# Kernel tuning notes

Hardware: AMD Instinct MI355X
Metric: run time of the kernel (lower is better)

## Reference

```python
import jax, jax.numpy as jnp
import numpy as np
from jax import lax

DN = ('NCHW', 'OIHW', 'NCHW')


def _conv(x, w, pad):
    return lax.conv_general_dilated(x, w, (1, 1), [(pad, pad), (pad, pad)], dimension_numbers=DN)


def _bn(x, gamma, beta, mean, var, eps=1e-5):
    inv = gamma * lax.rsqrt(var + eps)
    return x * inv[None, :, None, None] + (beta - mean * inv)[None, :, None, None]


def _unfold(x, K, pad):
    # torch.nn.Unfold layout: channel-major, kernel positions fastest -> (B, C, K*K, H, W)
    B, C, H, W = x.shape
    p = lax.conv_general_dilated_patches(x, (K, K), (1, 1), [(pad, pad), (pad, pad)], dimension_numbers=DN)
    return p.reshape(B, C, K * K, H, W)


def setup_inputs() -> dict:
    key = jax.random.key(0)
    ks = jax.random.split(key, 16)
    B, C, H, W, K = 16, 64, 64, 64, 3
    d = {
        'x': jax.random.normal(ks[0], (B, C, H, W), jnp.float32),
        'wq': jax.random.normal(ks[1], (C, C, 1, 1), jnp.float32) * 0.1,
        'wk': jax.random.normal(ks[2], (C, C, K, K), jnp.float32) * 0.05,
        'wv': jax.random.normal(ks[3], (C, C, 1, 1), jnp.float32) * 0.1,
        'pos_h': jax.random.normal(ks[4], (C, K, 1), jnp.float32),
        'pos_w': jax.random.normal(ks[5], (C, 1, K), jnp.float32),
    }
    for i, nm in enumerate(['q', 'k', 'v', 'o']):
        d[nm + '_gamma'] = jnp.ones((C,), jnp.float32)
        d[nm + '_beta'] = jnp.zeros((C,), jnp.float32)
        d[nm + '_mean'] = jax.random.normal(ks[6 + i], (C,), jnp.float32) * 0.1
        d[nm + '_var'] = jax.random.uniform(ks[10 + i], (C,), jnp.float32, 0.5, 1.5)
    return d


def reference(x, wq, q_gamma, q_beta, q_mean, q_var,
              wk, k_gamma, k_beta, k_mean, k_var,
              wv, v_gamma, v_beta, v_mean, v_var,
              pos_h, pos_w, o_gamma, o_beta, o_mean, o_var):
    B, C, H, W = x.shape
    K = pos_h.shape[1]
    heads = C // 8
    cph = C // heads  # channels per head

    q = jax.nn.relu(_bn(_conv(x, wq, 0), q_gamma, q_beta, q_mean, q_var))
    k = jax.nn.relu(_bn(_conv(x, wk, K // 2), k_gamma, k_beta, k_mean, k_var))
    v = _bn(_conv(x, wv, 0), v_gamma, v_beta, v_mean, v_var)

    # local keys + positional bias: (B, C, K*K, H, W)
    unfold_k = _unfold(k, K, K // 2)
    pos = (pos_h + pos_w).reshape(1, C, K * K, 1, 1)
    kp = (unfold_k + pos).reshape(B, heads, cph, K * K, H, W)
    qh = q.reshape(B, heads, cph, 1, H, W)

    attn = (qh * kp).sum(axis=2)            # (B, heads, K*K, H, W)
    attn = jax.nn.softmax(attn, axis=2)

    # local aggregation (LocalConvolution): weights shared across cph channels per head
    uv = _unfold(v, K, (K - 1) // 2).reshape(B, heads, cph, K * K, H, W)
    out = (attn[:, :, None] * uv).sum(axis=3).reshape(B, C, H, W)

    out = jax.nn.relu(_bn(out, o_gamma, o_beta, o_mean, o_var))
    return out
```

## Files before the change

### kernel.cpp

```cpp
#include <hip/hip_runtime.h>
#include <hip/hip_bf16.h>
#include <math.h>

#define B_ 16
#define C_ 64
#define H_ 64
#define W_ 64
#define KSTEPS 18

typedef __attribute__((ext_vector_type(8))) short bf16x8;
typedef __attribute__((ext_vector_type(4))) short bf16x4;
typedef __attribute__((ext_vector_type(4))) float f32x4;

static __device__ __forceinline__ unsigned short f2b(float f) {
    __hip_bfloat16 h = __float2bfloat16(f);
    return *reinterpret_cast<unsigned short*>(&h);
}
static __device__ __forceinline__ float b2f(unsigned short u) {
    __hip_bfloat16 h;
    *reinterpret_cast<unsigned short*>(&h) = u;
    return __bfloat162float(h);
}

__global__ __launch_bounds__(64) void prep_kernel(
    const float* __restrict__ wq, const float* __restrict__ wk, const float* __restrict__ wv,
    const float* __restrict__ qg, const float* __restrict__ qb, const float* __restrict__ qm, const float* __restrict__ qv,
    const float* __restrict__ kg, const float* __restrict__ kb, const float* __restrict__ km, const float* __restrict__ kv,
    const float* __restrict__ vg, const float* __restrict__ vb, const float* __restrict__ vm, const float* __restrict__ vv,
    const float* __restrict__ og, const float* __restrict__ ob, const float* __restrict__ om, const float* __restrict__ ov,
    unsigned short* __restrict__ Wp, float* __restrict__ bnp)
{
    const int bid = blockIdx.x;
    const int lane = threadIdx.x;
    if (bid < 12 * KSTEPS) {
        const int mf = bid / KSTEPS;
        const int ks = bid % KSTEPS;
        const int r = lane & 15;
        bf16x8 u;
#pragma unroll
        for (int j = 0; j < 8; j++) {
            int k = ks * 32 + ((lane >> 4) << 3) + j;
            int tap = k >> 6;
            int c = k & 63;
            float w;
            if (mf < 4)      { int co = mf * 16 + r;        w = (tap == 4) ? wq[co * 64 + c] : 0.f; }
            else if (mf < 8) { int co = (mf - 4) * 16 + r;  w = wk[(co * 64 + c) * 9 + tap]; }
            else             { int co = (mf - 8) * 16 + r;  w = (tap == 4) ? wv[co * 64 + c] : 0.f; }
            u[j] = (short)f2b(w);
        }
        *reinterpret_cast<bf16x8*>(Wp + ((size_t)(mf * KSTEPS + ks) * 64 + lane) * 8) = u;
    } else {
        const int c = lane;
        const float* G[4] = {qg, kg, vg, og};
        const float* Bt[4] = {qb, kb, vb, ob};
        const float* M[4] = {qm, km, vm, om};
        const float* V[4] = {qv, kv, vv, ov};
#pragma unroll
        for (int p = 0; p < 4; p++) {
            float inv = G[p][c] * rsqrtf(V[p][c] + 1e-5f);
            bnp[p * 128 + c] = inv;
            bnp[p * 128 + 64 + c] = Bt[p][c] - M[p][c] * inv;
        }
    }
}

__global__ __launch_bounds__(256) void xt_kernel(
    const float* __restrict__ x, unsigned short* __restrict__ xt)
{
    __shared__ float ls[64][65];
    const int b = blockIdx.x >> 6;
    const int h = blockIdx.x & 63;
    const int tid = threadIdx.x;
    const int w = tid & 63;
    const int cg = tid >> 6;
#pragma unroll
    for (int cc = 0; cc < 16; cc++) {
        int c = cg * 16 + cc;
        ls[c][w] = x[((b * 64 + c) * 64 + h) * 64 + w];
    }
    __syncthreads();
    const int px = tid & 63;
    bf16x8 u0, u1;
#pragma unroll
    for (int j = 0; j < 8; j++) {
        u0[j] = (short)f2b(ls[cg * 16 + j][px]);
        u1[j] = (short)f2b(ls[cg * 16 + 8 + j][px]);
    }
    size_t base = ((size_t)((b * 64 + h) * 64 + px)) * 64 + cg * 16;
    *reinterpret_cast<bf16x8*>(xt + base) = u0;
    *reinterpret_cast<bf16x8*>(xt + base + 8) = u1;
}

#define KSM_OFF 0
#define VSM_OFF 25344
#define QSM_OFF 50688
__global__ __launch_bounds__(512, 2) void fused_kernel(
    const unsigned short* __restrict__ xt, const unsigned short* __restrict__ Wp,
    const float* __restrict__ bnp,
    const float* __restrict__ ph, const float* __restrict__ pw,
    float* __restrict__ out)
{
    __shared__ __align__(16) char smem[58880];
    __shared__ float bns[512];
    __shared__ float phs[192], pws[192];
    const int bid = blockIdx.x;
    const int b = bid >> 6;
    const int h = bid & 63;
    const int tid = threadIdx.x;

    for (int i = tid; i < 8 * 5 * 66; i += 512) {
        int ch   = i & 7;
        int rest = i >> 3;
        int col  = rest % 66;
        int dy   = rest / 66;
        int gh = h - 2 + dy, gw = col - 1;
        bf16x8 u = (bf16x8){0,0,0,0,0,0,0,0};
        if ((unsigned)gh < 64u && (unsigned)gw < 64u)
            u = *reinterpret_cast<const bf16x8*>(xt + ((size_t)((b * 64 + gh) * 64 + gw)) * 64 + ch * 8);
        *reinterpret_cast<bf16x8*>(smem + ch * 5280 + dy * 1056 + col * 16) = u;
    }
    bns[tid & 511] = bnp[tid & 511];
    if (tid < 192) { phs[tid] = ph[tid]; pws[tid] = pw[tid]; }
    __syncthreads();

    const int wid = tid >> 6, lane = tid & 63;
    const int mf = wid & 3, half = wid >> 2;
    const int t = lane & 15, q4 = lane >> 4;
    const int vb16 = q4 * 5280 + t * 16;

    const unsigned short* WpQ = Wp + (size_t)(mf * KSTEPS) * 512 + lane * 8;
    const unsigned short* WpK = Wp + (size_t)((4 + mf) * KSTEPS) * 512 + lane * 8;
    const unsigned short* WpV = Wp + (size_t)((8 + mf) * KSTEPS) * 512 + lane * 8;

    f32x4 acck[6], accv[6], accq[2];
#pragma unroll
    for (int n = 0; n < 6; n++) { acck[n] = (f32x4){0.f,0.f,0.f,0.f}; accv[n] = (f32x4){0.f,0.f,0.f,0.f}; }
    accq[0] = (f32x4){0.f,0.f,0.f,0.f}; accq[1] = (f32x4){0.f,0.f,0.f,0.f};

#pragma unroll
    for (int ks = 0; ks < KSTEPS; ks++) {
        const int tap = ks >> 1;
        const int dy = tap / 3, dx = tap - dy * 3;
        const int koff = (ks & 1) * 21120;
        bf16x8 bf[6];
#pragma unroll
        for (int n = 0; n < 6; n++) {
            const int n16 = (half * 6 + n) * 16;
            const int r = n16 >> 6;
            const int colw0 = n16 & 63;
            bf[n] = *reinterpret_cast<const bf16x8*>(
                smem + vb16 + koff + (r + dy) * 1056 + (colw0 + dx) * 16);
        }
        bf16x8 afk = *reinterpret_cast<const bf16x8*>(WpK + (size_t)ks * 512);
#pragma unroll
        for (int n = 0; n < 6; n++)
            acck[n] = __builtin_amdgcn_mfma_f32_16x16x32_bf16(afk, bf[n], acck[n], 0, 0, 0);
        if (ks == 8 || ks == 9) {
            bf16x8 afq = *reinterpret_cast<const bf16x8*>(WpQ + (size_t)ks * 512);
            bf16x8 afv = *reinterpret_cast<const bf16x8*>(WpV + (size_t)ks * 512);
#pragma unroll
            for (int n = 0; n < 6; n++)
                accv[n] = __builtin_amdgcn_mfma_f32_16x16x32_bf16(afv, bf[n], accv[n], 0, 0, 0);
            bf16x8 bq0 = half ? bf[0] : bf[4];
            bf16x8 bq1 = half ? bf[1] : bf[5];
            accq[0] = __builtin_amdgcn_mfma_f32_16x16x32_bf16(afq, bq0, accq[0], 0, 0, 0);
            accq[1] = __builtin_amdgcn_mfma_f32_16x16x32_bf16(afq, bq1, accq[1], 0, 0, 0);
        }
    }
    __syncthreads();

    const int c0 = mf * 16 + q4 * 4;
    const int ech = c0 >> 3;
    const int esub = (q4 & 1) * 8;
    {
        f32x4 invk  = *reinterpret_cast<const f32x4*>(&bns[128 + c0]);
        f32x4 biask = *reinterpret_cast<const f32x4*>(&bns[128 + 64 + c0]);
        f32x4 invv  = *reinterpret_cast<const f32x4*>(&bns[256 + c0]);
        f32x4 biasv = *reinterpret_cast<const f32x4*>(&bns[256 + 64 + c0]);
        const int ebase = ech * 3168 + esub + t * 16;
#pragma unroll
        for (int n = 0; n < 6; n++) {
            const int n16 = (half * 6 + n) * 16;
            const int r = n16 >> 6;
            const int colw0 = n16 & 63;
            bf16x4 pk, pv;
#pragma unroll
            for (int j = 0; j < 4; j++) {
                pk[j] = (short)f2b(fmaxf(acck[n][j] * invk[j] + biask[j], 0.f));
                pv[j] = (short)f2b(accv[n][j] * invv[j] + biasv[j]);
            }
            const int off = r * 1056 + (colw0 + 1) * 16;
            *reinterpret_cast<bf16x4*>(smem + KSM_OFF + ebase + off) = pk;
            *reinterpret_cast<bf16x4*>(smem + VSM_OFF + ebase + off) = pv;
        }
        f32x4 invq  = *reinterpret_cast<const f32x4*>(&bns[c0]);
        f32x4 biasq = *reinterpret_cast<const f32x4*>(&bns[64 + c0]);
        const int qb16 = QSM_OFF + ech * 1024 + esub + t * 16;
#pragma unroll
        for (int i = 0; i < 2; i++) {
            const int nq = 4 + half * 2 + i;
            bf16x4 pq;
#pragma unroll
            for (int j = 0; j < 4; j++)
                pq[j] = (short)f2b(fmaxf(accq[i][j] * invq[j] + biasq[j], 0.f));
            *reinterpret_cast<bf16x4*>(smem + qb16 + (nq & 3) * 256) = pq;
        }
    }
    __syncthreads();

    const bf16x8 z8 = (bf16x8){0,0,0,0,0,0,0,0};
    for (int i = tid; i < 96; i += 512) {
        int buf = i & 1;
        int j = i >> 1;
        int ch = j & 7;
        int jj = j >> 3;
        int col = (jj & 1) ? 65 : 0;
        int rr = jj >> 1;
        *reinterpret_cast<bf16x8*>(smem + (buf ? VSM_OFF : KSM_OFF)
                                   + ch * 3168 + rr * 1056 + col * 16) = z8;
    }
    int rbad = (h == 0) ? 0 : ((h == 63) ? 2 : -1);
    if (rbad >= 0) {
        for (int i = tid; i < 66 * 8 * 2; i += 512) {
            int buf = i & 1;
            int j = i >> 1;
            int ch = j & 7;
            int col = j >> 3;
            *reinterpret_cast<bf16x8*>(smem + (buf ? VSM_OFF : KSM_OFF)
                                       + ch * 3168 + rbad * 1056 + col * 16) = z8;
        }
    }
    __syncthreads();

    const int px = tid & 63;
    const int head = tid >> 6;
    const int cb = head * 8;
    const int abase = head * 3168 + px * 16;

    float qf[8];
    {
        bf16x8 q8 = *reinterpret_cast<const bf16x8*>(smem + QSM_OFF + head * 1024 + px * 16);
#pragma unroll
        for (int j = 0; j < 8; j++) qf[j] = b2f((unsigned short)q8[j]);
    }

    float A[3], Bx[3];
#pragma unroll
    for (int tt = 0; tt < 3; tt++) {
        float a = 0.f, bb = 0.f;
#pragma unroll
        for (int j = 0; j < 8; j++) {
            a  = fmaf(qf[j], phs[(cb + j) * 3 + tt], a);
            bb = fmaf(qf[j], pws[(cb + j) * 3 + tt], bb);
        }
        A[tt] = a; Bx[tt] = bb;
    }

    float logit[9];
#pragma unroll
    for (int dy = 0; dy < 3; dy++) {
#pragma unroll
        for (int dx = 0; dx < 3; dx++) {
            bf16x8 k8 = *reinterpret_cast<const bf16x8*>(
                smem + KSM_OFF + abase + dy * 1056 + dx * 16);
            float qk = 0.f;
#pragma unroll
            for (int j = 0; j < 8; j++) qk = fmaf(qf[j], b2f((unsigned short)k8[j]), qk);
            logit[dy * 3 + dx] = qk + A[dy] + Bx[dx];
        }
    }

    float mx = logit[0];
#pragma unroll
    for (int tt = 1; tt < 9; tt++) mx = fmaxf(mx, logit[tt]);
    float e[9], sum = 0.f;
#pragma unroll
    for (int tt = 0; tt < 9; tt++) { e[tt] = __expf(logit[tt] - mx); sum += e[tt]; }
    float inv = 1.f / sum;

    float o[8];
#pragma unroll
    for (int j = 0; j < 8; j++) o[j] = 0.f;
#pragma unroll
    for (int dy = 0; dy < 3; dy++) {
#pragma unroll
        for (int dx = 0; dx < 3; dx++) {
            bf16x8 v8 = *reinterpret_cast<const bf16x8*>(
                smem + VSM_OFF + abase + dy * 1056 + dx * 16);
            float w = e[dy * 3 + dx];
#pragma unroll
            for (int j = 0; j < 8; j++) o[j] = fmaf(w, b2f((unsigned short)v8[j]), o[j]);
        }
    }

#pragma unroll
    for (int j = 0; j < 8; j++) {
        int c = cb + j;
        float val = fmaxf(fmaf(o[j] * inv, bns[384 + c], bns[384 + 64 + c]), 0.f);
        out[((size_t)(b * C_ + c) * H_ + h) * W_ + px] = val;
    }
}

extern "C" void kernel_launch(void* const* d_in, const int* in_sizes, int n_in,
                              void* d_out, int out_size, void* d_ws, size_t ws_size,
                              hipStream_t stream)
{
    const float* x   = (const float*)d_in[0];
    const float* wq  = (const float*)d_in[1];
    const float* wk  = (const float*)d_in[2];
    const float* wv  = (const float*)d_in[3];
    const float* ph  = (const float*)d_in[4];
    const float* pw  = (const float*)d_in[5];
    const float* qg  = (const float*)d_in[6];
    const float* qb  = (const float*)d_in[7];
    const float* qm  = (const float*)d_in[8];
    const float* qv  = (const float*)d_in[9];
    const float* kg  = (const float*)d_in[10];
    const float* kb  = (const float*)d_in[11];
    const float* km  = (const float*)d_in[12];
    const float* kv  = (const float*)d_in[13];
    const float* vg  = (const float*)d_in[14];
    const float* vb  = (const float*)d_in[15];
    const float* vm  = (const float*)d_in[16];
    const float* vv  = (const float*)d_in[17];
    const float* og  = (const float*)d_in[18];
    const float* ob  = (const float*)d_in[19];
    const float* om  = (const float*)d_in[20];
    const float* ov  = (const float*)d_in[21];

    char* ws = (char*)d_ws;
    unsigned short* Wp = (unsigned short*)ws;
    float* bnp = (float*)(ws + 221184);
    unsigned short* xt = (unsigned short*)(ws + 223232);

    prep_kernel<<<12 * KSTEPS + 1, 64, 0, stream>>>(
        wq, wk, wv, qg, qb, qm, qv, kg, kb, km, kv, vg, vb, vm, vv,
        og, ob, om, ov, Wp, bnp);

    xt_kernel<<<B_ * H_, 256, 0, stream>>>(x, xt);

    fused_kernel<<<B_ * H_, 512, 0, stream>>>(xt, Wp, bnp, ph, pw, (float*)d_out);
}
```

Measured before the change: 151.8 us.

## Alias K and V shared-memory tiles to cut LDS footprint and raise occupancy

K and V epilogue tiles now share one LDS region. K is written first and the softmax weights are computed from it; after a barrier, V overwrites the same region for the aggregation. Out-of-range rows are zeroed inline during the write instead of in a separate pass. This shrinks shared memory from about 58KB to 42KB and raises the launch-bounds occupancy hint from 2 to 6 blocks, at the cost of an extra barrier and accv staying live in registers longer.

```diff
diff --git a/kernel.cpp b/kernel.cpp
--- a/kernel.cpp
+++ b/kernel.cpp
@@ -91,16 +91,14 @@
     *reinterpret_cast<bf16x8*>(xt + base + 8) = u1;
 }
 
-#define KSM_OFF 0
-#define VSM_OFF 25344
-#define QSM_OFF 50688
-__global__ __launch_bounds__(512, 2) void fused_kernel(
+#define QSM_OFF 25344
+__global__ __launch_bounds__(512, 6) void fused_kernel(
     const unsigned short* __restrict__ xt, const unsigned short* __restrict__ Wp,
     const float* __restrict__ bnp,
     const float* __restrict__ ph, const float* __restrict__ pw,
     float* __restrict__ out)
 {
-    __shared__ __align__(16) char smem[58880];
+    __shared__ __align__(16) char smem[42240];
     __shared__ float bns[512];
     __shared__ float phs[192], pws[192];
     const int bid = blockIdx.x;
@@ -172,26 +170,26 @@
     const int c0 = mf * 16 + q4 * 4;
     const int ech = c0 >> 3;
     const int esub = (q4 & 1) * 8;
+    const int ebase = ech * 3168 + esub + t * 16;
+    const bf16x8 z8 = (bf16x8){0,0,0,0,0,0,0,0};
+    const bf16x4 z4 = (bf16x4){0,0,0,0};
+
     {
         f32x4 invk  = *reinterpret_cast<const f32x4*>(&bns[128 + c0]);
         f32x4 biask = *reinterpret_cast<const f32x4*>(&bns[128 + 64 + c0]);
-        f32x4 invv  = *reinterpret_cast<const f32x4*>(&bns[256 + c0]);
-        f32x4 biasv = *reinterpret_cast<const f32x4*>(&bns[256 + 64 + c0]);
-        const int ebase = ech * 3168 + esub + t * 16;
 #pragma unroll
         for (int n = 0; n < 6; n++) {
             const int n16 = (half * 6 + n) * 16;
             const int r = n16 >> 6;
             const int colw0 = n16 & 63;
-            bf16x4 pk, pv;
-#pragma unroll
-            for (int j = 0; j < 4; j++) {
-                pk[j] = (short)f2b(fmaxf(acck[n][j] * invk[j] + biask[j], 0.f));
-                pv[j] = (short)f2b(accv[n][j] * invv[j] + biasv[j]);
+            const bool rowok = ((unsigned)(h - 1 + r) < 64u);
+            bf16x4 pk = z4;
+            if (rowok) {
+#pragma unroll
+                for (int j = 0; j < 4; j++)
+                    pk[j] = (short)f2b(fmaxf(acck[n][j] * invk[j] + biask[j], 0.f));
             }
-            const int off = r * 1056 + (colw0 + 1) * 16;
-            *reinterpret_cast<bf16x4*>(smem + KSM_OFF + ebase + off) = pk;
-            *reinterpret_cast<bf16x4*>(smem + VSM_OFF + ebase + off) = pv;
+            *reinterpret_cast<bf16x4*>(smem + ebase + r * 1056 + (colw0 + 1) * 16) = pk;
         }
         f32x4 invq  = *reinterpret_cast<const f32x4*>(&bns[c0]);
         f32x4 biasq = *reinterpret_cast<const f32x4*>(&bns[64 + c0]);
@@ -205,29 +203,12 @@
                 pq[j] = (short)f2b(fmaxf(accq[i][j] * invq[j] + biasq[j], 0.f));
             *reinterpret_cast<bf16x4*>(smem + qb16 + (nq & 3) * 256) = pq;
         }
-    }
-    __syncthreads();
-
-    const bf16x8 z8 = (bf16x8){0,0,0,0,0,0,0,0};
-    for (int i = tid; i < 96; i += 512) {
-        int buf = i & 1;
-        int j = i >> 1;
-        int ch = j & 7;
-        int jj = j >> 3;
-        int col = (jj & 1) ? 65 : 0;
-        int rr = jj >> 1;
-        *reinterpret_cast<bf16x8*>(smem + (buf ? VSM_OFF : KSM_OFF)
-                                   + ch * 3168 + rr * 1056 + col * 16) = z8;
-    }
-    int rbad = (h == 0) ? 0 : ((h == 63) ? 2 : -1);
-    if (rbad >= 0) {
-        for (int i = tid; i < 66 * 8 * 2; i += 512) {
-            int buf = i & 1;
-            int j = i >> 1;
-            int ch = j & 7;
-            int col = j >> 3;
-            *reinterpret_cast<bf16x8*>(smem + (buf ? VSM_OFF : KSM_OFF)
-                                       + ch * 3168 + rbad * 1056 + col * 16) = z8;
+        if (tid < 48) {
+            int ch = tid & 7;
+            int jj = tid >> 3;
+            int col = (jj & 1) ? 65 : 0;
+            int rr = jj >> 1;
+            *reinterpret_cast<bf16x8*>(smem + ch * 3168 + rr * 1056 + col * 16) = z8;
         }
     }
     __syncthreads();
@@ -237,46 +218,74 @@
     const int cb = head * 8;
     const int abase = head * 3168 + px * 16;
 
-    float qf[8];
+    float e[9], inv;
     {
+        float qf[8];
         bf16x8 q8 = *reinterpret_cast<const bf16x8*>(smem + QSM_OFF + head * 1024 + px * 16);
 #pragma unroll
         for (int j = 0; j < 8; j++) qf[j] = b2f((unsigned short)q8[j]);
-    }
-
-    float A[3], Bx[3];
-#pragma unroll
-    for (int tt = 0; tt < 3; tt++) {
-        float a = 0.f, bb = 0.f;
-#pragma unroll
-        for (int j = 0; j < 8; j++) {
-            a  = fmaf(qf[j], phs[(cb + j) * 3 + tt], a);
-            bb = fmaf(qf[j], pws[(cb + j) * 3 + tt], bb);
-        }
-        A[tt] = a; Bx[tt] = bb;
-    }
-
-    float logit[9];
-#pragma unroll
-    for (int dy = 0; dy < 3; dy++) {
-#pragma unroll
-        for (int dx = 0; dx < 3; dx++) {
-            bf16x8 k8 = *reinterpret_cast<const bf16x8*>(
-                smem + KSM_OFF + abase + dy * 1056 + dx * 16);
-            float qk = 0.f;
-#pragma unroll
-            for (int j = 0; j < 8; j++) qk = fmaf(qf[j], b2f((unsigned short)k8[j]), qk);
-            logit[dy * 3 + dx] = qk + A[dy] + Bx[dx];
-        }
-    }
-
-    float mx = logit[0];
-#pragma unroll
-    for (int tt = 1; tt < 9; tt++) mx = fmaxf(mx, logit[tt]);
-    float e[9], sum = 0.f;
-#pragma unroll
-    for (int tt = 0; tt < 9; tt++) { e[tt] = __expf(logit[tt] - mx); sum += e[tt]; }
-    float inv = 1.f / sum;
+
+        float A[3], Bx[3];
+#pragma unroll
+        for (int tt = 0; tt < 3; tt++) {
+            float a = 0.f, bb = 0.f;
+#pragma unroll
+            for (int j = 0; j < 8; j++) {
+                a  = fmaf(qf[j], phs[(cb + j) * 3 + tt], a);
+                bb = fmaf(qf[j], pws[(cb + j) * 3 + tt], bb);
+            }
+            A[tt] = a; Bx[tt] = bb;
+        }
+
+        float logit[9];
+#pragma unroll
+        for (int dy = 0; dy < 3; dy++) {
+#pragma unroll
+            for (int dx = 0; dx < 3; dx++) {
+                bf16x8 k8 = *reinterpret_cast<const bf16x8*>(
+                    smem + abase + dy * 1056 + dx * 16);
+                float qk = 0.f;
+#pragma unroll
+                for (int j = 0; j < 8; j++) qk = fmaf(qf[j], b2f((unsigned short)k8[j]), qk);
+                logit[dy * 3 + dx] = qk + A[dy] + Bx[dx];
+            }
+        }
+        float mx = logit[0];
+#pragma unroll
+        for (int tt = 1; tt < 9; tt++) mx = fmaxf(mx, logit[tt]);
+        float sum = 0.f;
+#pragma unroll
+        for (int tt = 0; tt < 9; tt++) { e[tt] = __expf(logit[tt] - mx); sum += e[tt]; }
+        inv = 1.f / sum;
+    }
+    __syncthreads();
+
+    {
+        f32x4 invv  = *reinterpret_cast<const f32x4*>(&bns[256 + c0]);
+        f32x4 biasv = *reinterpret_cast<const f32x4*>(&bns[256 + 64 + c0]);
+#pragma unroll
+        for (int n = 0; n < 6; n++) {
+            const int n16 = (half * 6 + n) * 16;
+            const int r = n16 >> 6;
+            const int colw0 = n16 & 63;
+            const bool rowok = ((unsigned)(h - 1 + r) < 64u);
+            bf16x4 pv = z4;
+            if (rowok) {
+#pragma unroll
+                for (int j = 0; j < 4; j++)
+                    pv[j] = (short)f2b(accv[n][j] * invv[j] + biasv[j]);
+            }
+            *reinterpret_cast<bf16x4*>(smem + ebase + r * 1056 + (colw0 + 1) * 16) = pv;
+        }
+        if (tid < 48) {
+            int ch = tid & 7;
+            int jj = tid >> 3;
+            int col = (jj & 1) ? 65 : 0;
+            int rr = jj >> 1;
+            *reinterpret_cast<bf16x8*>(smem + ch * 3168 + rr * 1056 + col * 16) = z8;
+        }
+    }
+    __syncthreads();
 
     float o[8];
 #pragma unroll
@@ -286,13 +295,12 @@
 #pragma unroll
         for (int dx = 0; dx < 3; dx++) {
             bf16x8 v8 = *reinterpret_cast<const bf16x8*>(
-                smem + VSM_OFF + abase + dy * 1056 + dx * 16);
+                smem + abase + dy * 1056 + dx * 16);
             float w = e[dy * 3 + dx];
 #pragma unroll
             for (int j = 0; j < 8; j++) o[j] = fmaf(w, b2f((unsigned short)v8[j]), o[j]);
         }
     }
-
 #pragma unroll
     for (int j = 0; j < 8; j++) {
         int c = cb + j;
```

Result: slower. 210.7 us (+38.8%).
